# Performance work log

Measured on AMD Instinct MI355X. Metric: run time of the kernel, lower is better.

## Reference

```python
import jax, jax.numpy as jnp
import numpy as np
from jax import lax


def _upsample2x(x):
    # PyTorch nn.Upsample(scale_factor=2, mode='bilinear', align_corners=False) on NCHW
    B, C, H, W = x.shape
    def idx_w(n):
        src = (jnp.arange(2 * n, dtype=jnp.float32) + 0.5) / 2.0 - 0.5
        src = jnp.clip(src, 0.0, n - 1)
        i0 = jnp.floor(src).astype(jnp.int32)
        i1 = jnp.minimum(i0 + 1, n - 1)
        t = src - i0.astype(jnp.float32)
        return i0, i1, t
    r0, r1, ty = idx_w(H)
    c0, c1, tx = idx_w(W)
    xr = x[:, :, r0, :] * (1.0 - ty)[None, None, :, None] + x[:, :, r1, :] * ty[None, None, :, None]
    return xr[:, :, :, c0] * (1.0 - tx) + xr[:, :, :, c1] * tx


def _disco_conv_s2(x, psi_idx, psi_val, w, b, hw):
    # DISCO spherical conv: irregular neighbor gather + quadrature-weighted basis
    # contraction, then small GEMM over (in_channels, kernel basis).
    B, C, H, W = x.shape
    xf = x.reshape(B, C, H * W)
    g = xf[:, :, psi_idx]                      # [B,C,P,N] irregular gather
    z = jnp.einsum('bcpn,kpn->bckp', g, psi_val)  # [B,C,K,P]
    y = jnp.einsum('bckp,ock->bop', z, w) + b[None, :, None]
    return y.reshape(B, w.shape[0], hw[0], hw[1])


def _conv2d_same(x, w, b):
    y = lax.conv_general_dilated(x, w, (1, 1), 'SAME',
                                 dimension_numbers=('NCHW', 'OIHW', 'NCHW'))
    return y + b[None, :, None, None]


def _srcnn(x, psi_idx, psi_val, wd, bd, cw2, cb2, cw3, cb3, hw):
    x = jax.nn.relu(_disco_conv_s2(x, psi_idx, psi_val, wd, bd, hw))
    x = jax.nn.relu(_conv2d_same(x, cw2, cb2))
    return _conv2d_same(x, cw3, cb3)


def setup_inputs() -> dict:
    key = jax.random.key(0)
    ks = jax.random.split(key, 16)
    H0, W0 = 90, 180
    P1 = (2 * H0) * (2 * W0)          # 64800
    P2 = (4 * H0) * (4 * W0)          # 259200
    K, NNZ, F = 9, 8, 64
    inp = {
        'x': jax.random.normal(ks[0], (4, 1, H0, W0), jnp.float32),
        'elev0': jax.random.normal(ks[1], (4, 1, 2 * H0, 2 * W0), jnp.float32),
        'elev1': jax.random.normal(ks[2], (4, 1, 4 * H0, 4 * W0), jnp.float32),
        'psi_idx1': jax.random.randint(ks[3], (P1, NNZ), 0, P1, jnp.int32),
        'psi_val1': jax.random.uniform(ks[4], (K, P1, NNZ), jnp.float32) * 0.1,
        'w1': jax.random.normal(ks[5], (F, 2, K), jnp.float32) * 0.1,
        'b1': jnp.zeros((F,), jnp.float32),
        'cw2_1': jax.random.normal(ks[6], (F // 2, F, 5, 5), jnp.float32) * 0.02,
        'cb2_1': jnp.zeros((F // 2,), jnp.float32),
        'cw3_1': jax.random.normal(ks[7], (1, F // 2, 5, 5), jnp.float32) * 0.02,
        'cb3_1': jnp.zeros((1,), jnp.float32),
        'psi_idx2': jax.random.randint(ks[8], (P2, NNZ), 0, P2, jnp.int32),
        'psi_val2': jax.random.uniform(ks[9], (K, P2, NNZ), jnp.float32) * 0.1,
        'w2': jax.random.normal(ks[10], (F, 2, K), jnp.float32) * 0.1,
        'b2': jnp.zeros((F,), jnp.float32),
        'cw2_2': jax.random.normal(ks[11], (F // 2, F, 5, 5), jnp.float32) * 0.02,
        'cb2_2': jnp.zeros((F // 2,), jnp.float32),
        'cw3_2': jax.random.normal(ks[12], (1, F // 2, 5, 5), jnp.float32) * 0.02,
        'cb3_2': jnp.zeros((1,), jnp.float32),
    }
    return inp


def reference(x, elev0, elev1, psi_idx1, psi_val1, w1, b1, cw2_1, cb2_1, cw3_1, cb3_1,
              psi_idx2, psi_val2, w2, b2, cw2_2, cb2_2, cw3_2, cb3_2):
    h = _upsample2x(x)
    h = jnp.concatenate([h, elev0], axis=1)
    h = _srcnn(h, psi_idx1, psi_val1, w1, b1, cw2_1, cb2_1, cw3_1, cb3_1, (180, 360))
    # Stage 2
    h = _upsample2x(h)
    h = jnp.concatenate([h, elev1], axis=1)
    h = _srcnn(h, psi_idx2, psi_val2, w2, b2, cw2_2, cb2_2, cw3_2, cb3_2, (360, 720))
    return h
```

## Files before the change

### kernel.cpp

```cpp
#include <hip/hip_runtime.h>
#include <hip/hip_bf16.h>

typedef __hip_bfloat16 bf16;
typedef __attribute__((ext_vector_type(8))) short short8;
typedef __attribute__((ext_vector_type(4))) short short4v;
typedef __attribute__((ext_vector_type(4))) float float4v;

__device__ __forceinline__ short f2bs(float x) {
    bf16 b = __float2bfloat16(x);
    return *reinterpret_cast<short*>(&b);
}

__global__ void upsample_pack_k(const float* __restrict__ in,
                                const float* __restrict__ elev,
                                float* __restrict__ out2, int B, int H, int W) {
    const int OH = 2 * H, OW = 2 * W;
    const long total = (long)B * OH * OW;
    long i = (long)blockIdx.x * blockDim.x + threadIdx.x;
    if (i >= total) return;
    int ox = (int)(i % OW);
    long r = i / OW;
    int oy = (int)(r % OH);
    int b  = (int)(r / OH);
    float sy = fminf(fmaxf(oy * 0.5f - 0.25f, 0.0f), (float)(H - 1));
    float sx = fminf(fmaxf(ox * 0.5f - 0.25f, 0.0f), (float)(W - 1));
    int y0 = (int)sy; float ty = sy - (float)y0; int y1 = min(y0 + 1, H - 1);
    int x0 = (int)sx; float tx = sx - (float)x0; int x1 = min(x0 + 1, W - 1);
    const float* p = in + (size_t)b * H * W;
    float v00 = p[(size_t)y0 * W + x0];
    float v01 = p[(size_t)y0 * W + x1];
    float v10 = p[(size_t)y1 * W + x0];
    float v11 = p[(size_t)y1 * W + x1];
    float v = (v00 * (1.f - ty) + v10 * ty) * (1.f - tx)
            + (v01 * (1.f - ty) + v11 * ty) * tx;
    float2 o; o.x = v; o.y = elev[i];
    *(float2*)(out2 + i * 2) = o;
}

__global__ void wpack2_k(const float* __restrict__ src, short* __restrict__ dst) {
    int i = blockIdx.x * 256 + threadIdx.x;
    if (i >= 51200) return;
    int j    = i & 7;
    int r    = i >> 3;
    int lane = r & 63;
    int r2   = r >> 6;
    int mt   = r2 & 1;
    int r3   = r2 >> 1;
    int tap  = r3 % 25;
    int icc  = r3 / 25;
    int m = lane & 15, q = lane >> 4;
    int oc = mt * 16 + m;
    int ic = icc * 32 + q * 8 + j;
    dst[i] = f2bs(src[((size_t)oc * 64 + ic) * 25 + tap]);
}

__global__ void wpack3_k(const float* __restrict__ src, short* __restrict__ dst) {
    int i = blockIdx.x * 256 + threadIdx.x;
    if (i >= 12800) return;
    int j    = i & 7;
    int r    = i >> 3;
    int lane = r & 63;
    int tap  = r >> 6;
    int m = lane & 15, q = lane >> 4;
    dst[i] = (m == 0) ? f2bs(src[(size_t)(q * 8 + j) * 25 + tap]) : (short)0;
}

__global__ void wpackD_k(const float* __restrict__ w, short* __restrict__ dst) {
    int i = blockIdx.x * 256 + threadIdx.x;
    if (i >= 2048) return;
    int j = i & 7;
    int r = i >> 3;
    int lane = r & 63;
    int mtile = r >> 6;
    int q = lane >> 4, mm = lane & 15;
    int oc = mtile * 16 + mm;
    int k = q * 8 + j;
    dst[i] = (k < 18) ? f2bs(w[oc * 18 + k]) : (short)0;
}

__global__ __launch_bounds__(256)
void disco_k(const float* __restrict__ ui,
             const int* __restrict__ psi_idx, const float* __restrict__ psi_val,
             const short* __restrict__ wfragD, const float* __restrict__ bias,
             short* __restrict__ outh, int P) {
    __shared__ short zs[256 * 40];
    const int tid  = threadIdx.x;
    const int lane = tid & 63;
    const int wv   = tid >> 6;
    const int q    = lane >> 4;
    const int n    = lane & 15;

    for (int c0 = 0; c0 < 40; c0 += 8) *(short8*)(zs + tid * 40 + c0) = (short8)0;

    short8 af[4];
    float brg[4][4];
    #pragma unroll
    for (int mt = 0; mt < 4; mt++) {
        af[mt] = *(const short8*)(wfragD + ((mt * 64 + lane) << 3));
        #pragma unroll
        for (int r = 0; r < 4; r++) brg[mt][r] = bias[mt * 16 + q * 4 + r];
    }

    const int p = blockIdx.x * 256 + tid;
    const bool valid = p < P;

    int idx[8];
    float pv[9][8];
    if (valid) {
        const int* ip = psi_idx + (size_t)p * 8;
        int4 ia = *(const int4*)ip;
        int4 ib = *(const int4*)(ip + 4);
        idx[0]=ia.x; idx[1]=ia.y; idx[2]=ia.z; idx[3]=ia.w;
        idx[4]=ib.x; idx[5]=ib.y; idx[6]=ib.z; idx[7]=ib.w;
        #pragma unroll
        for (int k = 0; k < 9; k++) {
            const float* qp = psi_val + ((size_t)k * P + p) * 8;
            float4 qa = *(const float4*)qp;
            float4 qb = *(const float4*)(qp + 4);
            pv[k][0]=qa.x; pv[k][1]=qa.y; pv[k][2]=qa.z; pv[k][3]=qa.w;
            pv[k][4]=qb.x; pv[k][5]=qb.y; pv[k][6]=qb.z; pv[k][7]=qb.w;
        }
    }

    for (int bq = 0; bq < 4; bq++) {
        if (valid) {
            const float* ub = ui + (size_t)bq * P * 2;
            float g0[8], g1[8];
            #pragma unroll
            for (int t = 0; t < 8; t++) {
                float2 g = *(const float2*)(ub + (size_t)idx[t] * 2);
                g0[t] = g.x; g1[t] = g.y;
            }
            float z[18];
            #pragma unroll
            for (int j = 0; j < 18; j++) z[j] = 0.f;
            #pragma unroll
            for (int k = 0; k < 9; k++) {
                #pragma unroll
                for (int t = 0; t < 8; t++) {
                    z[k]     = fmaf(g0[t], pv[k][t], z[k]);
                    z[9 + k] = fmaf(g1[t], pv[k][t], z[9 + k]);
                }
            }
            #pragma unroll
            for (int c0i = 0; c0i < 16; c0i += 4) {
                short4v t4;
                t4.x = f2bs(z[c0i]); t4.y = f2bs(z[c0i+1]);
                t4.z = f2bs(z[c0i+2]); t4.w = f2bs(z[c0i+3]);
                *(short4v*)(zs + tid * 40 + c0i) = t4;
            }
            unsigned int lo = (unsigned short)f2bs(z[16]);
            unsigned int hi = (unsigned short)f2bs(z[17]);
            *(unsigned int*)(zs + tid * 40 + 16) = lo | (hi << 16);
        }
        __syncthreads();

        #pragma unroll
        for (int t = 0; t < 4; t++) {
            const int nt  = wv * 4 + t;
            const int pix = blockIdx.x * 256 + nt * 16 + n;
            short8 bz = *(const short8*)(zs + (nt * 16 + n) * 40 + q * 8);
            const bool pok = pix < P;
            short* hp = outh + ((size_t)bq * P + pix) * 64;
            #pragma unroll
            for (int mt = 0; mt < 4; mt++) {
                float4v acc = {0.f, 0.f, 0.f, 0.f};
                acc = __builtin_amdgcn_mfma_f32_16x16x32_bf16(af[mt], bz, acc, 0, 0, 0);
                if (pok) {
                    short4v o;
                    o.x = f2bs(fmaxf(acc.x + brg[mt][0], 0.f));
                    o.y = f2bs(fmaxf(acc.y + brg[mt][1], 0.f));
                    o.z = f2bs(fmaxf(acc.z + brg[mt][2], 0.f));
                    o.w = f2bs(fmaxf(acc.w + brg[mt][3], 0.f));
                    *(short4v*)(hp + mt * 16 + q * 4) = o;
                }
            }
        }
        __syncthreads();
    }
}

__global__ __launch_bounds__(256, 2)
void conv2_k(const short* __restrict__ hS, const short* __restrict__ wfrag,
             const float* __restrict__ bias, short* __restrict__ outc,
             int H, int W) {
    __shared__ short slab[8 * 68 * 40];
    const int tid  = threadIdx.x;
    const int wv   = tid >> 6;
    const int lane = tid & 63;
    const int q    = lane >> 4;
    const int n    = lane & 15;
    const int xbase = blockIdx.x * 64;
    const int ybase = blockIdx.y * 4;
    const int b     = blockIdx.z;
    const short* hb = hS + (size_t)b * H * W * 64;

    float4v acc[4][2];
    #pragma unroll
    for (int nt = 0; nt < 4; nt++)
        #pragma unroll
        for (int mt = 0; mt < 2; mt++)
            acc[nt][mt] = (float4v){0.f, 0.f, 0.f, 0.f};

    float brg[2][4];
    #pragma unroll
    for (int mt = 0; mt < 2; mt++)
        #pragma unroll
        for (int r = 0; r < 4; r++) brg[mt][r] = bias[mt * 16 + q * 4 + r];

    for (int icc = 0; icc < 2; icc++) {
        __syncthreads();
        for (int l = tid; l < 2176; l += 256) {
            int qq  = l & 3;
            int pix = l >> 2;
            int row = pix / 68;
            int col = pix - row * 68;
            int gy = ybase - 2 + row;
            int gx = xbase - 2 + col;
            short8 v = (short8)0;
            if ((unsigned)gy < (unsigned)H && (unsigned)gx < (unsigned)W)
                v = *(const short8*)(hb + ((size_t)gy * W + gx) * 64 + icc * 32 + qq * 8);
            *(short8*)(slab + pix * 40 + qq * 8) = v;
        }
        __syncthreads();

        const short* wfr = wfrag + (size_t)icc * 25600;
        #pragma unroll
        for (int ky = 0; ky < 5; ky++) {
            #pragma unroll
            for (int kx = 0; kx < 5; kx++) {
                const int tap = ky * 5 + kx;
                short8 wf0 = *(const short8*)(wfr + ((tap * 2 + 0) * 64 + lane) * 8);
                short8 wf1 = *(const short8*)(wfr + ((tap * 2 + 1) * 64 + lane) * 8);
                const int boff = ((wv + ky) * 68 + n + kx) * 40 + q * 8;
                #pragma unroll
                for (int nt = 0; nt < 4; nt++) {
                    short8 bfr = *(const short8*)(slab + boff + nt * 640);
                    acc[nt][0] = __builtin_amdgcn_mfma_f32_16x16x32_bf16(wf0, bfr, acc[nt][0], 0, 0, 0);
                    acc[nt][1] = __builtin_amdgcn_mfma_f32_16x16x32_bf16(wf1, bfr, acc[nt][1], 0, 0, 0);
                }
            }
        }
    }

    const int y = ybase + wv;
    #pragma unroll
    for (int nt = 0; nt < 4; nt++) {
        const int x = xbase + nt * 16 + n;
        if (x < W) {
            short* cp = outc + (((size_t)b * H * W + (size_t)y * W + x) * 32);
            #pragma unroll
            for (int mt = 0; mt < 2; mt++) {
                short4v o;
                o.x = f2bs(fmaxf(acc[nt][mt].x + brg[mt][0], 0.f));
                o.y = f2bs(fmaxf(acc[nt][mt].y + brg[mt][1], 0.f));
                o.z = f2bs(fmaxf(acc[nt][mt].z + brg[mt][2], 0.f));
                o.w = f2bs(fmaxf(acc[nt][mt].w + brg[mt][3], 0.f));
                *(short4v*)(cp + mt * 16 + q * 4) = o;
            }
        }
    }
}

__global__ __launch_bounds__(256, 2)
void conv3_k(const short* __restrict__ cP, const short* __restrict__ wf3,
             const float* __restrict__ bias, float* __restrict__ out,
             int H, int W) {
    __shared__ short slab[8 * 68 * 40];
    const int tid  = threadIdx.x;
    const int wv   = tid >> 6;
    const int lane = tid & 63;
    const int q    = lane >> 4;
    const int n    = lane & 15;
    const int xbase = blockIdx.x * 64;
    const int ybase = blockIdx.y * 4;
    const int b     = blockIdx.z;
    const short* cb = cP + (size_t)b * H * W * 32;

    for (int l = tid; l < 2176; l += 256) {
        int qq  = l & 3;
        int pix = l >> 2;
        int row = pix / 68;
        int col = pix - row * 68;
        int gy = ybase - 2 + row;
        int gx = xbase - 2 + col;
        short8 v = (short8)0;
        if ((unsigned)gy < (unsigned)H && (unsigned)gx < (unsigned)W)
            v = *(const short8*)(cb + ((size_t)gy * W + gx) * 32 + qq * 8);
        *(short8*)(slab + pix * 40 + qq * 8) = v;
    }
    __syncthreads();

    float4v acc[4];
    #pragma unroll
    for (int nt = 0; nt < 4; nt++) acc[nt] = (float4v){0.f, 0.f, 0.f, 0.f};

    #pragma unroll
    for (int ky = 0; ky < 5; ky++) {
        #pragma unroll
        for (int kx = 0; kx < 5; kx++) {
            const int tap = ky * 5 + kx;
            short8 a = *(const short8*)(wf3 + ((size_t)(tap * 64 + lane)) * 8);
            const int boff = ((wv + ky) * 68 + n + kx) * 40 + q * 8;
            #pragma unroll
            for (int nt = 0; nt < 4; nt++) {
                short8 bfr = *(const short8*)(slab + boff + nt * 640);
                acc[nt] = __builtin_amdgcn_mfma_f32_16x16x32_bf16(a, bfr, acc[nt], 0, 0, 0);
            }
        }
    }

    const int y = ybase + wv;
    const float bi = bias[0];
    if (q == 0 && y < H) {
        #pragma unroll
        for (int nt = 0; nt < 4; nt++) {
            const int x = xbase + nt * 16 + n;
            if (x < W) out[((size_t)b * H + y) * W + x] = acc[nt].x + bi;
        }
    }
}

extern "C" void kernel_launch(void* const* d_in, const int* in_sizes, int n_in,
                              void* d_out, int out_size, void* d_ws, size_t ws_size,
                              hipStream_t stream) {
    const float* x        = (const float*)d_in[0];
    const float* elev0    = (const float*)d_in[1];
    const float* elev1    = (const float*)d_in[2];
    const int*   psi_idx1 = (const int*)  d_in[3];
    const float* psi_val1 = (const float*)d_in[4];
    const float* w1       = (const float*)d_in[5];
    const float* b1       = (const float*)d_in[6];
    const float* cw2_1    = (const float*)d_in[7];
    const float* cb2_1    = (const float*)d_in[8];
    const float* cw3_1    = (const float*)d_in[9];
    const float* cb3_1    = (const float*)d_in[10];
    const int*   psi_idx2 = (const int*)  d_in[11];
    const float* psi_val2 = (const float*)d_in[12];
    const float* w2       = (const float*)d_in[13];
    const float* b2       = (const float*)d_in[14];
    const float* cw2_2    = (const float*)d_in[15];
    const float* cb2_2    = (const float*)d_in[16];
    const float* cw3_2    = (const float*)d_in[17];
    const float* cb3_2    = (const float*)d_in[18];

    const int B = 4;
    const int H1 = 180, W1 = 360, P1 = H1 * W1;
    const int H2 = 360, W2 = 720, P2 = H2 * W2;

    char* ws = (char*)d_ws;
    short* h    = (short*)(ws);
    short* c    = (short*)(ws + 132710400);
    float* u2i  = (float*)(ws + 149299200);
    float* u1i  = (float*)(ws + 199065600);
    float* s1   = (float*)(ws + 201139200);
    short* wfA  = (short*)(ws + 202176000);
    short* wfB  = (short*)(ws + 202278400);
    short* wfD1 = (short*)(ws + 202380800);
    short* wfD2 = (short*)(ws + 202384896);
    short* wf31 = (short*)(ws + 202388992);
    short* wf32 = (short*)(ws + 202414592);
    (void)ws_size; (void)in_sizes; (void)n_in; (void)out_size;

    wpack2_k<<<(51200 + 255) / 256, 256, 0, stream>>>(cw2_1, wfA);
    wpack2_k<<<(51200 + 255) / 256, 256, 0, stream>>>(cw2_2, wfB);
    wpack3_k<<<(12800 + 255) / 256, 256, 0, stream>>>(cw3_1, wf31);
    wpack3_k<<<(12800 + 255) / 256, 256, 0, stream>>>(cw3_2, wf32);
    wpackD_k<<<8, 256, 0, stream>>>(w1, wfD1);
    wpackD_k<<<8, 256, 0, stream>>>(w2, wfD2);

    upsample_pack_k<<<(B * P1 + 255) / 256, 256, 0, stream>>>(x, elev0, u1i, B, 90, 180);
    disco_k<<<(P1 + 255) / 256, 256, 0, stream>>>(
        u1i, psi_idx1, psi_val1, wfD1, b1, h, P1);
    conv2_k<<<dim3((W1 + 63) / 64, H1 / 4, B), 256, 0, stream>>>(
        h, wfA, cb2_1, c, H1, W1);
    conv3_k<<<dim3((W1 + 63) / 64, H1 / 4, B), 256, 0, stream>>>(
        c, wf31, cb3_1, s1, H1, W1);

    upsample_pack_k<<<(B * P2 + 255) / 256, 256, 0, stream>>>(s1, elev1, u2i, B, H1, W1);
    disco_k<<<(P2 + 255) / 256, 256, 0, stream>>>(
        u2i, psi_idx2, psi_val2, wfD2, b2, h, P2);
    conv2_k<<<dim3((W2 + 63) / 64, H2 / 4, B), 256, 0, stream>>>(
        h, wfB, cb2_2, c, H2, W2);
    conv3_k<<<dim3((W2 + 63) / 64, H2 / 4, B), 256, 0, stream>>>(
        c, wf32, cb3_2, (float*)d_out, H2, W2);
}
```

Measured before the change: 556.4 us.

## Compute two output rows per wave in 5x5 convs and merge weight-pack kernels

The conv2 and conv3 kernels now cover 8 output rows per block, with each wave computing two adjacent rows. Every B fragment loaded from the shared-memory slab is reused for both rows, which cuts LDS reads and the halo-load overhead per output pixel. The cost is twice the accumulator registers and a larger shared slab, which can lower occupancy. The six weight-packing launches are also merged into one kernel to save launch overhead.

Measured after the change: 542.9 us. 1.02x faster.

```diff
diff --git a/kernel.cpp b/kernel.cpp
--- a/kernel.cpp
+++ b/kernel.cpp
@@ -37,45 +37,54 @@
     *(float2*)(out2 + i * 2) = o;
 }
 
-__global__ void wpack2_k(const float* __restrict__ src, short* __restrict__ dst) {
-    int i = blockIdx.x * 256 + threadIdx.x;
-    if (i >= 51200) return;
-    int j    = i & 7;
-    int r    = i >> 3;
-    int lane = r & 63;
-    int r2   = r >> 6;
-    int mt   = r2 & 1;
-    int r3   = r2 >> 1;
-    int tap  = r3 % 25;
-    int icc  = r3 / 25;
-    int m = lane & 15, q = lane >> 4;
-    int oc = mt * 16 + m;
-    int ic = icc * 32 + q * 8 + j;
-    dst[i] = f2bs(src[((size_t)oc * 64 + ic) * 25 + tap]);
-}
-
-__global__ void wpack3_k(const float* __restrict__ src, short* __restrict__ dst) {
-    int i = blockIdx.x * 256 + threadIdx.x;
-    if (i >= 12800) return;
-    int j    = i & 7;
-    int r    = i >> 3;
-    int lane = r & 63;
-    int tap  = r >> 6;
-    int m = lane & 15, q = lane >> 4;
-    dst[i] = (m == 0) ? f2bs(src[(size_t)(q * 8 + j) * 25 + tap]) : (short)0;
-}
-
-__global__ void wpackD_k(const float* __restrict__ w, short* __restrict__ dst) {
-    int i = blockIdx.x * 256 + threadIdx.x;
-    if (i >= 2048) return;
-    int j = i & 7;
-    int r = i >> 3;
-    int lane = r & 63;
-    int mtile = r >> 6;
-    int q = lane >> 4, mm = lane & 15;
-    int oc = mtile * 16 + mm;
-    int k = q * 8 + j;
-    dst[i] = (k < 18) ? f2bs(w[oc * 18 + k]) : (short)0;
+__global__ void packall_k(const float* __restrict__ cw2_1, const float* __restrict__ cw2_2,
+                          const float* __restrict__ cw3_1, const float* __restrict__ cw3_2,
+                          const float* __restrict__ w1,    const float* __restrict__ w2,
+                          short* __restrict__ wfA,  short* __restrict__ wfB,
+                          short* __restrict__ wf31, short* __restrict__ wf32,
+                          short* __restrict__ wfD1, short* __restrict__ wfD2) {
+    int gi = blockIdx.x * 256 + threadIdx.x;
+    if (gi < 102400) {
+        const float* src = (gi < 51200) ? cw2_1 : cw2_2;
+        short* dst       = (gi < 51200) ? wfA   : wfB;
+        int i = (gi < 51200) ? gi : gi - 51200;
+        int j    = i & 7;
+        int r    = i >> 3;
+        int lane = r & 63;
+        int r2   = r >> 6;
+        int mt   = r2 & 1;
+        int r3   = r2 >> 1;
+        int tap  = r3 % 25;
+        int icc  = r3 / 25;
+        int m = lane & 15, q = lane >> 4;
+        int oc = mt * 16 + m;
+        int ic = icc * 32 + q * 8 + j;
+        dst[i] = f2bs(src[((size_t)oc * 64 + ic) * 25 + tap]);
+    } else if (gi < 128000) {
+        int gi2 = gi - 102400;
+        const float* src = (gi2 < 12800) ? cw3_1 : cw3_2;
+        short* dst       = (gi2 < 12800) ? wf31  : wf32;
+        int i = (gi2 < 12800) ? gi2 : gi2 - 12800;
+        int j    = i & 7;
+        int r    = i >> 3;
+        int lane = r & 63;
+        int tap  = r >> 6;
+        int m = lane & 15, q = lane >> 4;
+        dst[i] = (m == 0) ? f2bs(src[(size_t)(q * 8 + j) * 25 + tap]) : (short)0;
+    } else if (gi < 132096) {
+        int gi2 = gi - 128000;
+        const float* src = (gi2 < 2048) ? w1 : w2;
+        short* dst       = (gi2 < 2048) ? wfD1 : wfD2;
+        int i = (gi2 < 2048) ? gi2 : gi2 - 2048;
+        int j = i & 7;
+        int r = i >> 3;
+        int lane = r & 63;
+        int mtile = r >> 6;
+        int q = lane >> 4, mm = lane & 15;
+        int oc = mtile * 16 + mm;
+        int k = q * 8 + j;
+        dst[i] = (k < 18) ? f2bs(src[oc * 18 + k]) : (short)0;
+    }
 }
 
 __global__ __launch_bounds__(256)
@@ -184,23 +193,25 @@
 void conv2_k(const short* __restrict__ hS, const short* __restrict__ wfrag,
              const float* __restrict__ bias, short* __restrict__ outc,
              int H, int W) {
-    __shared__ short slab[8 * 68 * 40];
+    __shared__ short slab[12 * 68 * 40];
     const int tid  = threadIdx.x;
     const int wv   = tid >> 6;
     const int lane = tid & 63;
     const int q    = lane >> 4;
     const int n    = lane & 15;
     const int xbase = blockIdx.x * 64;
-    const int ybase = blockIdx.y * 4;
+    const int ybase = blockIdx.y * 8;
     const int b     = blockIdx.z;
     const short* hb = hS + (size_t)b * H * W * 64;
 
-    float4v acc[4][2];
-    #pragma unroll
-    for (int nt = 0; nt < 4; nt++)
-        #pragma unroll
-        for (int mt = 0; mt < 2; mt++)
-            acc[nt][mt] = (float4v){0.f, 0.f, 0.f, 0.f};
+    float4v acc[2][4][2];
+    #pragma unroll
+    for (int ri = 0; ri < 2; ri++)
+        #pragma unroll
+        for (int nt = 0; nt < 4; nt++)
+            #pragma unroll
+            for (int mt = 0; mt < 2; mt++)
+                acc[ri][nt][mt] = (float4v){0.f, 0.f, 0.f, 0.f};
 
     float brg[2][4];
     #pragma unroll
@@ -210,7 +221,7 @@
 
     for (int icc = 0; icc < 2; icc++) {
         __syncthreads();
-        for (int l = tid; l < 2176; l += 256) {
+        for (int l = tid; l < 3264; l += 256) {
             int qq  = l & 3;
             int pix = l >> 2;
             int row = pix / 68;
@@ -226,37 +237,57 @@
 
         const short* wfr = wfrag + (size_t)icc * 25600;
         #pragma unroll
-        for (int ky = 0; ky < 5; ky++) {
+        for (int t = 0; t < 6; t++) {
+            const int srow = wv * 2 + t;
             #pragma unroll
             for (int kx = 0; kx < 5; kx++) {
-                const int tap = ky * 5 + kx;
-                short8 wf0 = *(const short8*)(wfr + ((tap * 2 + 0) * 64 + lane) * 8);
-                short8 wf1 = *(const short8*)(wfr + ((tap * 2 + 1) * 64 + lane) * 8);
-                const int boff = ((wv + ky) * 68 + n + kx) * 40 + q * 8;
+                short8 w0a, w0b, w1a, w1b;
+                if (t <= 4) {
+                    const int tp = t * 5 + kx;
+                    w0a = *(const short8*)(wfr + ((tp * 2 + 0) * 64 + lane) * 8);
+                    w0b = *(const short8*)(wfr + ((tp * 2 + 1) * 64 + lane) * 8);
+                }
+                if (t >= 1) {
+                    const int tp = (t - 1) * 5 + kx;
+                    w1a = *(const short8*)(wfr + ((tp * 2 + 0) * 64 + lane) * 8);
+                    w1b = *(const short8*)(wfr + ((tp * 2 + 1) * 64 + lane) * 8);
+                }
+                const int boff = (srow * 68 + n + kx) * 40 + q * 8;
                 #pragma unroll
                 for (int nt = 0; nt < 4; nt++) {
                     short8 bfr = *(const short8*)(slab + boff + nt * 640);
-                    acc[nt][0] = __builtin_amdgcn_mfma_f32_16x16x32_bf16(wf0, bfr, acc[nt][0], 0, 0, 0);
-                    acc[nt][1] = __builtin_amdgcn_mfma_f32_16x16x32_bf16(wf1, bfr, acc[nt][1], 0, 0, 0);
-                }
-            }
-        }
-    }
-
-    const int y = ybase + wv;
-    #pragma unroll
-    for (int nt = 0; nt < 4; nt++) {
-        const int x = xbase + nt * 16 + n;
-        if (x < W) {
-            short* cp = outc + (((size_t)b * H * W + (size_t)y * W + x) * 32);
-            #pragma unroll
-            for (int mt = 0; mt < 2; mt++) {
-                short4v o;
-                o.x = f2bs(fmaxf(acc[nt][mt].x + brg[mt][0], 0.f));
-                o.y = f2bs(fmaxf(acc[nt][mt].y + brg[mt][1], 0.f));
-                o.z = f2bs(fmaxf(acc[nt][mt].z + brg[mt][2], 0.f));
-                o.w = f2bs(fmaxf(acc[nt][mt].w + brg[mt][3], 0.f));
-                *(short4v*)(cp + mt * 16 + q * 4) = o;
+                    if (t <= 4) {
+                        acc[0][nt][0] = __builtin_amdgcn_mfma_f32_16x16x32_bf16(w0a, bfr, acc[0][nt][0], 0, 0, 0);
+                        acc[0][nt][1] = __builtin_amdgcn_mfma_f32_16x16x32_bf16(w0b, bfr, acc[0][nt][1], 0, 0, 0);
+                    }
+                    if (t >= 1) {
+                        acc[1][nt][0] = __builtin_amdgcn_mfma_f32_16x16x32_bf16(w1a, bfr, acc[1][nt][0], 0, 0, 0);
+                        acc[1][nt][1] = __builtin_amdgcn_mfma_f32_16x16x32_bf16(w1b, bfr, acc[1][nt][1], 0, 0, 0);
+                    }
+                }
+            }
+        }
+    }
+
+    #pragma unroll
+    for (int ri = 0; ri < 2; ri++) {
+        const int y = ybase + wv * 2 + ri;
+        if (y < H) {
+            #pragma unroll
+            for (int nt = 0; nt < 4; nt++) {
+                const int x = xbase + nt * 16 + n;
+                if (x < W) {
+                    short* cp = outc + (((size_t)b * H * W + (size_t)y * W + x) * 32);
+                    #pragma unroll
+                    for (int mt = 0; mt < 2; mt++) {
+                        short4v o;
+                        o.x = f2bs(fmaxf(acc[ri][nt][mt].x + brg[mt][0], 0.f));
+                        o.y = f2bs(fmaxf(acc[ri][nt][mt].y + brg[mt][1], 0.f));
+                        o.z = f2bs(fmaxf(acc[ri][nt][mt].z + brg[mt][2], 0.f));
+                        o.w = f2bs(fmaxf(acc[ri][nt][mt].w + brg[mt][3], 0.f));
+                        *(short4v*)(cp + mt * 16 + q * 4) = o;
+                    }
+                }
             }
         }
     }
@@ -266,18 +297,18 @@
 void conv3_k(const short* __restrict__ cP, const short* __restrict__ wf3,
              const float* __restrict__ bias, float* __restrict__ out,
              int H, int W) {
-    __shared__ short slab[8 * 68 * 40];
+    __shared__ short slab[12 * 68 * 40];
     const int tid  = threadIdx.x;
     const int wv   = tid >> 6;
     const int lane = tid & 63;
     const int q    = lane >> 4;
     const int n    = lane & 15;
     const int xbase = blockIdx.x * 64;
-    const int ybase = blockIdx.y * 4;
+    const int ybase = blockIdx.y * 8;
     const int b     = blockIdx.z;
     const short* cb = cP + (size_t)b * H * W * 32;
 
-    for (int l = tid; l < 2176; l += 256) {
+    for (int l = tid; l < 3264; l += 256) {
         int qq  = l & 3;
         int pix = l >> 2;
         int row = pix / 68;
@@ -291,32 +322,42 @@
     }
     __syncthreads();
 
-    float4v acc[4];
-    #pragma unroll
-    for (int nt = 0; nt < 4; nt++) acc[nt] = (float4v){0.f, 0.f, 0.f, 0.f};
-
-    #pragma unroll
-    for (int ky = 0; ky < 5; ky++) {
+    float4v acc[2][4];
+    #pragma unroll
+    for (int ri = 0; ri < 2; ri++)
+        #pragma unroll
+        for (int nt = 0; nt < 4; nt++) acc[ri][nt] = (float4v){0.f, 0.f, 0.f, 0.f};
+
+    #pragma unroll
+    for (int t = 0; t < 6; t++) {
+        const int srow = wv * 2 + t;
         #pragma unroll
         for (int kx = 0; kx < 5; kx++) {
-            const int tap = ky * 5 + kx;
-            short8 a = *(const short8*)(wf3 + ((size_t)(tap * 64 + lane)) * 8);
-            const int boff = ((wv + ky) * 68 + n + kx) * 40 + q * 8;
+            short8 a0, a1;
+            if (t <= 4) a0 = *(const short8*)(wf3 + (((t * 5 + kx) * 64 + lane)) * 8);
+            if (t >= 1) a1 = *(const short8*)(wf3 + ((((t - 1) * 5 + kx) * 64 + lane)) * 8);
+            const int boff = (srow * 68 + n + kx) * 40 + q * 8;
             #pragma unroll
             for (int nt = 0; nt < 4; nt++) {
                 short8 bfr = *(const short8*)(slab + boff + nt * 640);
-                acc[nt] = __builtin_amdgcn_mfma_f32_16x16x32_bf16(a, bfr, acc[nt], 0, 0, 0);
-            }
-        }
-    }
-
-    const int y = ybase + wv;
+                if (t <= 4) acc[0][nt] = __builtin_amdgcn_mfma_f32_16x16x32_bf16(a0, bfr, acc[0][nt], 0, 0, 0);
+                if (t >= 1) acc[1][nt] = __builtin_amdgcn_mfma_f32_16x16x32_bf16(a1, bfr, acc[1][nt], 0, 0, 0);
+            }
+        }
+    }
+
     const float bi = bias[0];
-    if (q == 0 && y < H) {
-        #pragma unroll
-        for (int nt = 0; nt < 4; nt++) {
-            const int x = xbase + nt * 16 + n;
-            if (x < W) out[((size_t)b * H + y) * W + x] = acc[nt].x + bi;
+    if (q == 0) {
+        #pragma unroll
+        for (int ri = 0; ri < 2; ri++) {
+            const int y = ybase + wv * 2 + ri;
+            if (y < H) {
+                #pragma unroll
+                for (int nt = 0; nt < 4; nt++) {
+                    const int x = xbase + nt * 16 + n;
+                    if (x < W) out[((size_t)b * H + y) * W + x] = acc[ri][nt].x + bi;
+                }
+            }
         }
     }
 }
@@ -362,26 +403,22 @@
     short* wf32 = (short*)(ws + 202414592);
     (void)ws_size; (void)in_sizes; (void)n_in; (void)out_size;
 
-    wpack2_k<<<(51200 + 255) / 256, 256, 0, stream>>>(cw2_1, wfA);
-    wpack2_k<<<(51200 + 255) / 256, 256, 0, stream>>>(cw2_2, wfB);
-    wpack3_k<<<(12800 + 255) / 256, 256, 0, stream>>>(cw3_1, wf31);
-    wpack3_k<<<(12800 + 255) / 256, 256, 0, stream>>>(cw3_2, wf32);
-    wpackD_k<<<8, 256, 0, stream>>>(w1, wfD1);
-    wpackD_k<<<8, 256, 0, stream>>>(w2, wfD2);
+    packall_k<<<(132096 + 255) / 256, 256, 0, stream>>>(
+        cw2_1, cw2_2, cw3_1, cw3_2, w1, w2, wfA, wfB, wf31, wf32, wfD1, wfD2);
 
     upsample_pack_k<<<(B * P1 + 255) / 256, 256, 0, stream>>>(x, elev0, u1i, B, 90, 180);
     disco_k<<<(P1 + 255) / 256, 256, 0, stream>>>(
         u1i, psi_idx1, psi_val1, wfD1, b1, h, P1);
-    conv2_k<<<dim3((W1 + 63) / 64, H1 / 4, B), 256, 0, stream>>>(
+    conv2_k<<<dim3((W1 + 63) / 64, (H1 + 7) / 8, B), 256, 0, stream>>>(
         h, wfA, cb2_1, c, H1, W1);
-    conv3_k<<<dim3((W1 + 63) / 64, H1 / 4, B), 256, 0, stream>>>(
+    conv3_k<<<dim3((W1 + 63) / 64, (H1 + 7) / 8, B), 256, 0, stream>>>(
         c, wf31, cb3_1, s1, H1, W1);
 
     upsample_pack_k<<<(B * P2 + 255) / 256, 256, 0, stream>>>(s1, elev1, u2i, B, H1, W1);
     disco_k<<<(P2 + 255) / 256, 256, 0, stream>>>(
         u2i, psi_idx2, psi_val2, wfD2, b2, h, P2);
-    conv2_k<<<dim3((W2 + 63) / 64, H2 / 4, B), 256, 0, stream>>>(
+    conv2_k<<<dim3((W2 + 63) / 64, (H2 + 7) / 8, B), 256, 0, stream>>>(
         h, wfB, cb2_2, c, H2, W2);
-    conv3_k<<<dim3((W2 + 63) / 64, H2 / 4, B), 256, 0, stream>>>(
+    conv3_k<<<dim3((W2 + 63) / 64, (H2 + 7) / 8, B), 256, 0, stream>>>(
         c, wf32, cb3_2, (float*)d_out, H2, W2);
 }
```
